# Optimization experiments

Hardware: AMD Instinct MI355X
Metric: run time of the kernel (lower is better)

The kernel has to match this reference:

```python
import math
import jax, jax.numpy as jnp
import numpy as np

NUM_HEADS = 16
QUERY_SIZE = 1024
SEQ = 2048
HEAD = QUERY_SIZE // NUM_HEADS  # qk_size = vo_size = 64


def setup_inputs() -> dict:
    key = jax.random.key(0)
    ks = jax.random.split(key, 8)
    s = 0.02
    query = jax.random.normal(ks[0], (SEQ, QUERY_SIZE), jnp.float32)
    key_ = jax.random.normal(ks[1], (SEQ, QUERY_SIZE), jnp.float32)
    value = jax.random.normal(ks[2], (SEQ, QUERY_SIZE), jnp.float32)
    # causal mask (mask='causal' with state=None -> offset 0)
    mask = jnp.tril(jnp.ones((SEQ, SEQ), dtype=bool))
    Wq = jax.random.normal(ks[3], (QUERY_SIZE, QUERY_SIZE), jnp.float32) * s
    Wk = jax.random.normal(ks[4], (QUERY_SIZE, QUERY_SIZE), jnp.float32) * s
    Wv = jax.random.normal(ks[5], (QUERY_SIZE, QUERY_SIZE), jnp.float32) * s
    Wo = jax.random.normal(ks[6], (QUERY_SIZE, QUERY_SIZE), jnp.float32) * s
    return {"query": query, "key_": key_, "value": value, "mask": mask,
            "Wq": Wq, "Wk": Wk, "Wv": Wv, "Wo": Wo}


def reference(query, key_, value, mask, Wq, Wk, Wv, Wo):
    H, D = NUMS = NUM_HEADS, HEAD
    S = query.shape[0]
    inv_sqrt_d = 1.0 / math.sqrt(D)
    # per-token linear projections, split into heads: [S, H, D]
    q = (query @ Wq.T).reshape(S, H, D)
    k = (key_ @ Wk.T).reshape(S, H, D)
    v = (value @ Wv.T).reshape(S, H, D)
    # NOTE: original divides BOTH q and k by sqrt(d) (effective 1/d scaling)
    q = q * inv_sqrt_d
    k = k * inv_sqrt_d
    # logits per head: [H, S, S]
    logits = jnp.einsum('shd,Shd->hsS', q, k)
    logits = jnp.where(mask[None, :, :], logits, jnp.finfo(logits.dtype).min)
    # per-head GLOBAL max subtraction, softmax in fp32, cast back (faithful)
    m = jnp.max(logits, axis=(1, 2), keepdims=True)
    weights = jax.nn.softmax((logits - m).astype(jnp.float32), axis=-1).astype(query.dtype)
    attn = jnp.einsum('hsS,ShD->shD', weights, v).reshape(S, H * D)
    return attn @ Wo.T
```

## Files before the change

### kernel.cpp

```cpp
#include <hip/hip_runtime.h>
#include <hip/hip_bf16.h>

typedef __bf16 bf16_t;
typedef __bf16 bf16x8 __attribute__((ext_vector_type(8)));
typedef float f32x4 __attribute__((ext_vector_type(4)));

#define MFMA(A, B, C) __builtin_amdgcn_mfma_f32_16x16x32_bf16(A, B, C, 0, 0, 0)

#define GLL16(g, l) __builtin_amdgcn_global_load_lds(                      \
    (const __attribute__((address_space(1))) void*)(g),                    \
    (__attribute__((address_space(3))) void*)(l), 16, 0, 0)

__global__ __launch_bounds__(256) void cvt_all(
    const float* __restrict__ q, const float* __restrict__ k, const float* __restrict__ v,
    const float* __restrict__ wq, const float* __restrict__ wk,
    const float* __restrict__ wv, const float* __restrict__ wo,
    bf16_t* __restrict__ xq, bf16_t* __restrict__ xk, bf16_t* __restrict__ xv,
    bf16_t* __restrict__ ywq, bf16_t* __restrict__ ywk,
    bf16_t* __restrict__ ywv, bf16_t* __restrict__ ywo)
{
  const long gid = (long)blockIdx.x * 256 + threadIdx.x;
  const float* s; bf16_t* d; long off; float sc = 1.0f;
  if (gid < 262144)       { s = q;  d = xq;  off = gid; }
  else if (gid < 524288)  { s = k;  d = xk;  off = gid - 262144; }
  else if (gid < 786432)  { s = v;  d = xv;  off = gid - 524288; }
  else if (gid < 917504)  { s = wq; d = ywq; off = gid - 786432;  sc = 0.125f; }
  else if (gid < 1048576) { s = wk; d = ywk; off = gid - 917504;  sc = 0.125f; }
  else if (gid < 1179648) { s = wv; d = ywv; off = gid - 1048576; }
  else                    { s = wo; d = ywo; off = gid - 1179648; }
  const float* p = s + off * 8;
  float4 a = *(const float4*)p, b = *(const float4*)(p + 4);
  bf16x8 o;
  o[0] = (bf16_t)(a.x * sc); o[1] = (bf16_t)(a.y * sc);
  o[2] = (bf16_t)(a.z * sc); o[3] = (bf16_t)(a.w * sc);
  o[4] = (bf16_t)(b.x * sc); o[5] = (bf16_t)(b.y * sc);
  o[6] = (bf16_t)(b.z * sc); o[7] = (bf16_t)(b.w * sc);
  *(bf16x8*)(d + off * 8) = o;
}

__device__ __forceinline__ void gemm_core(const bf16_t* __restrict__ A,
                                          const bf16_t* __restrict__ W,
                                          int bm, int bn,
                                          bf16_t (&As)[2][128 * 64],
                                          bf16_t (&Bs)[2][64 * 64],
                                          f32x4 (&acc)[4][2])
{
  const int tid = threadIdx.x, lane = tid & 63, wave = tid >> 6;
  const int l15 = lane & 15, l4 = lane >> 4, l7 = l15 & 7;
  const int wm = (wave >> 1) * 64, wn = (wave & 1) * 32;

  auto stage = [&](int buf, int k0) {
#pragma unroll
    for (int i = 0; i < 4; ++i) {
      const int id = i * 256 + tid, row = id >> 3, cph = id & 7;
      GLL16(A + (size_t)(bm + row) * 1024 + k0 + 8 * (cph ^ (row & 7)),
            &As[buf][(i * 256 + wave * 64) * 8]);
    }
#pragma unroll
    for (int i = 0; i < 2; ++i) {
      const int id = i * 256 + tid, row = id >> 3, cph = id & 7;
      GLL16(W + (size_t)(bn + row) * 1024 + k0 + 8 * (cph ^ (row & 7)),
            &Bs[buf][(i * 256 + wave * 64) * 8]);
    }
  };

  stage(0, 0);
#pragma unroll
  for (int s = 0; s < 16; ++s) {
    __syncthreads();
    if (s + 1 < 16) stage((s + 1) & 1, (s + 1) * 64);
    const bf16_t* as = As[s & 1];
    const bf16_t* bs = Bs[s & 1];
#pragma unroll
    for (int ks = 0; ks < 2; ++ks) {
      bf16x8 af[4], bfr[2];
#pragma unroll
      for (int i = 0; i < 4; ++i)
        af[i] = *(const bf16x8*)(&as[(wm + i * 16 + l15) * 64 + 8 * ((ks * 4 + l4) ^ l7)]);
#pragma unroll
      for (int j = 0; j < 2; ++j)
        bfr[j] = *(const bf16x8*)(&bs[(wn + j * 16 + l15) * 64 + 8 * ((ks * 4 + l4) ^ l7)]);
#pragma unroll
      for (int i = 0; i < 4; ++i)
#pragma unroll
        for (int j = 0; j < 2; ++j)
          acc[i][j] = MFMA(af[i], bfr[j], acc[i][j]);
    }
  }
}

__global__ __launch_bounds__(256) void gemm_qkv(
    const bf16_t* __restrict__ xq, const bf16_t* __restrict__ xk, const bf16_t* __restrict__ xv,
    const bf16_t* __restrict__ ywq, const bf16_t* __restrict__ ywk, const bf16_t* __restrict__ ywv,
    bf16_t* __restrict__ qo, bf16_t* __restrict__ ko, bf16_t* __restrict__ vt)
{
  __shared__ __align__(16) bf16_t As[2][128 * 64];
  __shared__ __align__(16) bf16_t Bs[2][64 * 64];
  const int z = blockIdx.z;
  const bf16_t* A = z == 0 ? xq : z == 1 ? xk : xv;
  const bf16_t* W = z == 0 ? ywq : z == 1 ? ywk : ywv;
  const int bm = blockIdx.x * 128, bn = blockIdx.y * 64;
  f32x4 acc[4][2] = {};
  gemm_core(A, W, bm, bn, As, Bs, acc);
  const int tid = threadIdx.x, lane = tid & 63, wave = tid >> 6;
  const int l15 = lane & 15, l4 = lane >> 4;
  const int wm = (wave >> 1) * 64, wn = (wave & 1) * 32;
  if (z < 2) {
    bf16_t* C = z == 0 ? qo : ko;
#pragma unroll
    for (int i = 0; i < 4; ++i)
#pragma unroll
      for (int j = 0; j < 2; ++j)
#pragma unroll
        for (int r = 0; r < 4; ++r)
          C[(size_t)(bm + wm + i * 16 + 4 * l4 + r) * 1024 + bn + wn + j * 16 + l15] =
              (bf16_t)acc[i][j][r];
  } else {
#pragma unroll
    for (int i = 0; i < 4; ++i)
#pragma unroll
      for (int j = 0; j < 2; ++j)
#pragma unroll
        for (int r = 0; r < 4; ++r)
          vt[(size_t)(bn + wn + j * 16 + l15) * 2048 + bm + wm + i * 16 + 4 * l4 + r] =
              (bf16_t)acc[i][j][r];
  }
}

__global__ __launch_bounds__(256) void gemm_out(
    const bf16_t* __restrict__ ctx, const bf16_t* __restrict__ ywo, float* __restrict__ out)
{
  __shared__ __align__(16) bf16_t As[2][128 * 64];
  __shared__ __align__(16) bf16_t Bs[2][64 * 64];
  const int bm = blockIdx.x * 128, bn = blockIdx.y * 64;
  f32x4 acc[4][2] = {};
  gemm_core(ctx, ywo, bm, bn, As, Bs, acc);
  const int tid = threadIdx.x, lane = tid & 63, wave = tid >> 6;
  const int l15 = lane & 15, l4 = lane >> 4;
  const int wm = (wave >> 1) * 64, wn = (wave & 1) * 32;
#pragma unroll
  for (int i = 0; i < 4; ++i)
#pragma unroll
    for (int j = 0; j < 2; ++j)
#pragma unroll
      for (int r = 0; r < 4; ++r)
        out[(size_t)(bm + wm + i * 16 + 4 * l4 + r) * 1024 + bn + wn + j * 16 + l15] =
            acc[i][j][r];
}

__global__ __launch_bounds__(512) void attn512(
    const bf16_t* __restrict__ Qb, const bf16_t* __restrict__ Kb,
    const bf16_t* __restrict__ Vt, bf16_t* __restrict__ Ctx)
{
  __shared__ __align__(16) bf16_t Ks[2][128 * 64];
  __shared__ __align__(16) bf16_t Vs[2][64 * 128];
  __shared__ __align__(16) bf16_t Ps[8][16 * 64];

  const int bid = blockIdx.x;
  const int h = 2 * (bid & 7) + ((bid >> 3) >> 4);
  const int jp = (bid >> 3) & 15;
  const int hoff = h * 64;
  const int tid = threadIdx.x;
  const int lane = tid & 63, wave = tid >> 6;
  const int g = wave & 3, kh = wave >> 2;
  const int l15 = lane & 15, l4 = lane >> 4;
  const int l7 = l15 & 7;

  const int qtA = jp, qtB = 31 - jp;
  const int qbA = qtA * 64, qbB = qtB * 64;
  const int nscA = qtA / 2 + 1, nscB = qtB / 2 + 1;

  const int qrA = qbA + g * 16 + l15, qrB = qbB + g * 16 + l15;
  bf16x8 qA0 = *(const bf16x8*)(Qb + (size_t)qrA * 1024 + hoff + 8 * l4);
  bf16x8 qA1 = *(const bf16x8*)(Qb + (size_t)qrA * 1024 + hoff + 32 + 8 * l4);
  bf16x8 qB0 = *(const bf16x8*)(Qb + (size_t)qrB * 1024 + hoff + 8 * l4);
  bf16x8 qB1 = *(const bf16x8*)(Qb + (size_t)qrB * 1024 + hoff + 32 + 8 * l4);

  f32x4 oA[4] = {}, oB[4] = {};
  float dA[4] = {0.f, 0.f, 0.f, 0.f}, dB[4] = {0.f, 0.f, 0.f, 0.f};

  bf16x8 rk[2], rv[2];
  auto issue = [&](int sc) {
    const int t0 = sc * 128;
#pragma unroll
    for (int i = 0; i < 2; ++i) {
      const int id = tid + 512 * i;
      const int kr = id >> 3, kc = id & 7;
      rk[i] = *(const bf16x8*)(Kb + (size_t)(t0 + kr) * 1024 + hoff + 8 * kc);
      const int vr = id >> 4, vc = id & 15;
      rv[i] = *(const bf16x8*)(Vt + (size_t)(hoff + vr) * 2048 + t0 + 8 * vc);
    }
  };
  auto commit = [&](int buf) {
#pragma unroll
    for (int i = 0; i < 2; ++i) {
      const int id = tid + 512 * i;
      const int kr = id >> 3, kc = id & 7;
      *(bf16x8*)(&Ks[buf][kr * 64 + 8 * (kc ^ (kr & 7))]) = rk[i];
      const int vr = id >> 4, vc = id & 15;
      *(bf16x8*)(&Vs[buf][vr * 128 + 8 * (vc ^ (vr & 7))]) = rv[i];
    }
  };

  auto process = [&](int sc, int cur, int qb, const bf16x8& q0, const bf16x8& q1,
                     f32x4 (&oacc)[4], float (&den)[4]) {
    if (128 * sc + 64 * kh > qb + g * 16 + 15) return;
    const int tb = 128 * sc + 64 * kh;
#pragma unroll
    for (int sub = 0; sub < 4; ++sub) {
      const int krow = 64 * kh + 16 * sub + l15;
      bf16x8 kf0 = *(const bf16x8*)(&Ks[cur][krow * 64 + 8 * (l4 ^ l7)]);
      bf16x8 kf1 = *(const bf16x8*)(&Ks[cur][krow * 64 + 8 * ((4 + l4) ^ l7)]);
      __builtin_amdgcn_s_setprio(1);
      f32x4 sv = {};
      sv = MFMA(q0, kf0, sv);
      sv = MFMA(q1, kf1, sv);
      __builtin_amdgcn_s_setprio(0);
      const int t = tb + 16 * sub + l15;
#pragma unroll
      for (int r = 0; r < 4; ++r) {
        const int qq = qb + g * 16 + 4 * l4 + r;
        const float p = (t <= qq) ? __expf(sv[r]) : 0.0f;
        const bf16_t pb = (bf16_t)p;
        den[r] += (float)pb;
        const int prow = 4 * l4 + r;
        const int pch = 2 * sub + (l15 >> 3);
        Ps[wave][prow * 64 + 8 * (pch ^ (prow & 7)) + l7] = pb;
      }
    }
    asm volatile("s_waitcnt lgkmcnt(0)" ::: "memory");
    __builtin_amdgcn_s_setprio(1);
#pragma unroll
    for (int ks = 0; ks < 2; ++ks) {
      bf16x8 pf = *(const bf16x8*)(&Ps[wave][l15 * 64 + 8 * ((ks * 4 + l4) ^ l7)]);
#pragma unroll
      for (int db = 0; db < 4; ++db) {
        bf16x8 vf = *(const bf16x8*)(&Vs[cur][(db * 16 + l15) * 128 + 64 * kh + 8 * ((ks * 4 + l4) ^ l7)]);
        oacc[db] = MFMA(pf, vf, oacc[db]);
      }
    }
    __builtin_amdgcn_s_setprio(0);
  };

  issue(0);
  commit(0);
  int cur = 0;
  for (int sc = 0; sc < nscB; ++sc) {
    const bool pre = (sc + 1 < nscB);
    __syncthreads();
    if (pre) issue(sc + 1);
    process(sc, cur, qbB, qB0, qB1, oB, dB);
    if (sc < nscA) process(sc, cur, qbA, qA0, qA1, oA, dA);
    if (pre) commit(cur ^ 1);
    cur ^= 1;
  }

  __syncthreads();
#pragma unroll
  for (int r = 0; r < 4; ++r)
#pragma unroll
    for (int m = 1; m < 16; m <<= 1) {
      dA[r] += __shfl_xor(dA[r], m, 64);
      dB[r] += __shfl_xor(dB[r], m, 64);
    }
  float* Os = (float*)(&Ks[0][0]);
  float* Ds = (float*)(&Vs[0][0]);
  if (kh == 1) {
#pragma unroll
    for (int r = 0; r < 4; ++r) {
      const int row = g * 16 + 4 * l4 + r;
#pragma unroll
      for (int db = 0; db < 4; ++db) {
        Os[(0 * 64 + row) * 64 + db * 16 + l15] = oA[db][r];
        Os[(1 * 64 + row) * 64 + db * 16 + l15] = oB[db][r];
      }
      if (l15 == 0) { Ds[0 * 64 + row] = dA[r]; Ds[1 * 64 + row] = dB[r]; }
    }
  }
  __syncthreads();
  if (kh == 0) {
#pragma unroll
    for (int r = 0; r < 4; ++r) {
      const int row = g * 16 + 4 * l4 + r;
      const float iA = 1.0f / (dA[r] + Ds[0 * 64 + row]);
      const float iB = 1.0f / (dB[r] + Ds[1 * 64 + row]);
#pragma unroll
      for (int db = 0; db < 4; ++db) {
        const float vA = oA[db][r] + Os[(0 * 64 + row) * 64 + db * 16 + l15];
        const float vB = oB[db][r] + Os[(1 * 64 + row) * 64 + db * 16 + l15];
        Ctx[(size_t)(qbA + row) * 1024 + hoff + db * 16 + l15] = (bf16_t)(vA * iA);
        Ctx[(size_t)(qbB + row) * 1024 + hoff + db * 16 + l15] = (bf16_t)(vB * iB);
      }
    }
  }
}

extern "C" void kernel_launch(void* const* d_in, const int* in_sizes, int n_in,
                              void* d_out, int out_size, void* d_ws, size_t ws_size,
                              hipStream_t stream)
{
  const float* query = (const float*)d_in[0];
  const float* key_  = (const float*)d_in[1];
  const float* value = (const float*)d_in[2];
  const float* Wq = (const float*)d_in[4];
  const float* Wk = (const float*)d_in[5];
  const float* Wv = (const float*)d_in[6];
  const float* Wo = (const float*)d_in[7];
  float* out = (float*)d_out;

  const size_t SE = (size_t)2048 * 1024, EE = (size_t)1024 * 1024;
  bf16_t* xq  = (bf16_t*)d_ws;
  bf16_t* xk  = xq + SE;
  bf16_t* xv  = xk + SE;
  bf16_t* wq  = xv + SE;
  bf16_t* wk  = wq + EE;
  bf16_t* wv  = wk + EE;
  bf16_t* wo  = wv + EE;
  bf16_t* qo  = wo + EE;
  bf16_t* ko  = qo + SE;
  bf16_t* vt  = ko + SE;
  bf16_t* ctx = vt + SE;

  cvt_all<<<5120, 256, 0, stream>>>(query, key_, value, Wq, Wk, Wv, Wo,
                                    xq, xk, xv, wq, wk, wv, wo);
  gemm_qkv<<<dim3(16, 16, 3), 256, 0, stream>>>(xq, xk, xv, wq, wk, wv, qo, ko, vt);
  attn512<<<256, 512, 0, stream>>>(qo, ko, vt, ctx);
  gemm_out<<<dim3(16, 16), 256, 0, stream>>>(ctx, wo, out);
}
```

Before: 75.64 us.

## Use head-major Q/K/ctx layout and register-streamed attention without shared K/V tiles

Q, K and the attention context are stored head-major ([head][seq][64]) so each head's data is contiguous, and the output GEMM reads ctx in that layout. The attention kernel drops the shared-memory K/V double buffer and barriers. Each wave loads its own 32-key slice of K and V straight into registers, with two register sets alternating to prefetch. The four key-split partial results are combined through shared memory at the end, and the log2(e) factor is folded into Wk so exp2 replaces exp. This removes per-iteration block syncs and LDS staging, at the cost of more registers, uncoalesced per-lane global loads, and a larger final combine.

```diff
diff --git a/kernel.cpp b/kernel.cpp
--- a/kernel.cpp
+++ b/kernel.cpp
@@ -25,7 +25,7 @@
   else if (gid < 524288)  { s = k;  d = xk;  off = gid - 262144; }
   else if (gid < 786432)  { s = v;  d = xv;  off = gid - 524288; }
   else if (gid < 917504)  { s = wq; d = ywq; off = gid - 786432;  sc = 0.125f; }
-  else if (gid < 1048576) { s = wk; d = ywk; off = gid - 917504;  sc = 0.125f; }
+  else if (gid < 1048576) { s = wk; d = ywk; off = gid - 917504;  sc = 0.125f * 1.44269504f; }
   else if (gid < 1179648) { s = wv; d = ywv; off = gid - 1048576; }
   else                    { s = wo; d = ywo; off = gid - 1179648; }
   const float* p = s + off * 8;
@@ -38,6 +38,7 @@
   *(bf16x8*)(d + off * 8) = o;
 }
 
+template<int HM_A>
 __device__ __forceinline__ void gemm_core(const bf16_t* __restrict__ A,
                                           const bf16_t* __restrict__ W,
                                           int bm, int bn,
@@ -53,8 +54,10 @@
 #pragma unroll
     for (int i = 0; i < 4; ++i) {
       const int id = i * 256 + tid, row = id >> 3, cph = id & 7;
-      GLL16(A + (size_t)(bm + row) * 1024 + k0 + 8 * (cph ^ (row & 7)),
-            &As[buf][(i * 256 + wave * 64) * 8]);
+      const size_t asrc = HM_A
+          ? (size_t)(k0 >> 6) * 131072 + (size_t)(bm + row) * 64 + 8 * (cph ^ (row & 7))
+          : (size_t)(bm + row) * 1024 + k0 + 8 * (cph ^ (row & 7));
+      GLL16(A + asrc, &As[buf][(i * 256 + wave * 64) * 8]);
     }
 #pragma unroll
     for (int i = 0; i < 2; ++i) {
@@ -92,7 +95,7 @@
 __global__ __launch_bounds__(256) void gemm_qkv(
     const bf16_t* __restrict__ xq, const bf16_t* __restrict__ xk, const bf16_t* __restrict__ xv,
     const bf16_t* __restrict__ ywq, const bf16_t* __restrict__ ywk, const bf16_t* __restrict__ ywv,
-    bf16_t* __restrict__ qo, bf16_t* __restrict__ ko, bf16_t* __restrict__ vt)
+    bf16_t* __restrict__ qhm, bf16_t* __restrict__ khm, bf16_t* __restrict__ vt)
 {
   __shared__ __align__(16) bf16_t As[2][128 * 64];
   __shared__ __align__(16) bf16_t Bs[2][64 * 64];
@@ -101,19 +104,20 @@
   const bf16_t* W = z == 0 ? ywq : z == 1 ? ywk : ywv;
   const int bm = blockIdx.x * 128, bn = blockIdx.y * 64;
   f32x4 acc[4][2] = {};
-  gemm_core(A, W, bm, bn, As, Bs, acc);
+  gemm_core<0>(A, W, bm, bn, As, Bs, acc);
   const int tid = threadIdx.x, lane = tid & 63, wave = tid >> 6;
   const int l15 = lane & 15, l4 = lane >> 4;
   const int wm = (wave >> 1) * 64, wn = (wave & 1) * 32;
   if (z < 2) {
-    bf16_t* C = z == 0 ? qo : ko;
+    bf16_t* C = z == 0 ? qhm : khm;
+    const size_t hbase = (size_t)(bn >> 6) * 131072;
 #pragma unroll
     for (int i = 0; i < 4; ++i)
 #pragma unroll
       for (int j = 0; j < 2; ++j)
 #pragma unroll
         for (int r = 0; r < 4; ++r)
-          C[(size_t)(bm + wm + i * 16 + 4 * l4 + r) * 1024 + bn + wn + j * 16 + l15] =
+          C[hbase + (size_t)(bm + wm + i * 16 + 4 * l4 + r) * 64 + wn + j * 16 + l15] =
               (bf16_t)acc[i][j][r];
   } else {
 #pragma unroll
@@ -134,7 +138,7 @@
   __shared__ __align__(16) bf16_t Bs[2][64 * 64];
   const int bm = blockIdx.x * 128, bn = blockIdx.y * 64;
   f32x4 acc[4][2] = {};
-  gemm_core(ctx, ywo, bm, bn, As, Bs, acc);
+  gemm_core<1>(ctx, ywo, bm, bn, As, Bs, acc);
   const int tid = threadIdx.x, lane = tid & 63, wave = tid >> 6;
   const int l15 = lane & 15, l4 = lane >> 4;
   const int wm = (wave >> 1) * 64, wn = (wave & 1) * 32;
@@ -148,151 +152,161 @@
             acc[i][j][r];
 }
 
-__global__ __launch_bounds__(512) void attn512(
-    const bf16_t* __restrict__ Qb, const bf16_t* __restrict__ Kb,
-    const bf16_t* __restrict__ Vt, bf16_t* __restrict__ Ctx)
-{
-  __shared__ __align__(16) bf16_t Ks[2][128 * 64];
-  __shared__ __align__(16) bf16_t Vs[2][64 * 128];
-  __shared__ __align__(16) bf16_t Ps[8][16 * 64];
+__global__ __launch_bounds__(512) void attn_nb(
+    const bf16_t* __restrict__ Qh, const bf16_t* __restrict__ Kh,
+    const bf16_t* __restrict__ Vth, bf16_t* __restrict__ Ch)
+{
+  __shared__ __align__(16) bf16_t Ps[8][32 * 40];
+  __shared__ float Ocomb[3][2][32][66];
+  __shared__ float Dcomb[3][2][32];
 
   const int bid = blockIdx.x;
-  const int h = 2 * (bid & 7) + ((bid >> 3) >> 4);
+  const int h = 2 * (bid & 7) + (bid >> 7);
   const int jp = (bid >> 3) & 15;
-  const int hoff = h * 64;
-  const int tid = threadIdx.x;
-  const int lane = tid & 63, wave = tid >> 6;
-  const int g = wave & 3, kh = wave >> 2;
+  const int tid = threadIdx.x, lane = tid & 63, wave = tid >> 6;
+  const int qh = wave & 1, tq = wave >> 1;
   const int l15 = lane & 15, l4 = lane >> 4;
-  const int l7 = l15 & 7;
+
+  const bf16_t* Qb = Qh + (size_t)h * 131072;
+  const bf16_t* Kb = Kh + (size_t)h * 131072;
+  const bf16_t* Vb = Vth + (size_t)h * 131072;
 
   const int qtA = jp, qtB = 31 - jp;
   const int qbA = qtA * 64, qbB = qtB * 64;
-  const int nscA = qtA / 2 + 1, nscB = qtB / 2 + 1;
-
-  const int qrA = qbA + g * 16 + l15, qrB = qbB + g * 16 + l15;
-  bf16x8 qA0 = *(const bf16x8*)(Qb + (size_t)qrA * 1024 + hoff + 8 * l4);
-  bf16x8 qA1 = *(const bf16x8*)(Qb + (size_t)qrA * 1024 + hoff + 32 + 8 * l4);
-  bf16x8 qB0 = *(const bf16x8*)(Qb + (size_t)qrB * 1024 + hoff + 8 * l4);
-  bf16x8 qB1 = *(const bf16x8*)(Qb + (size_t)qrB * 1024 + hoff + 32 + 8 * l4);
-
-  f32x4 oA[4] = {}, oB[4] = {};
-  float dA[4] = {0.f, 0.f, 0.f, 0.f}, dB[4] = {0.f, 0.f, 0.f, 0.f};
-
-  bf16x8 rk[2], rv[2];
-  auto issue = [&](int sc) {
-    const int t0 = sc * 128;
-#pragma unroll
-    for (int i = 0; i < 2; ++i) {
-      const int id = tid + 512 * i;
-      const int kr = id >> 3, kc = id & 7;
-      rk[i] = *(const bf16x8*)(Kb + (size_t)(t0 + kr) * 1024 + hoff + 8 * kc);
-      const int vr = id >> 4, vc = id & 15;
-      rv[i] = *(const bf16x8*)(Vt + (size_t)(hoff + vr) * 2048 + t0 + 8 * vc);
-    }
-  };
-  auto commit = [&](int buf) {
-#pragma unroll
-    for (int i = 0; i < 2; ++i) {
-      const int id = tid + 512 * i;
-      const int kr = id >> 3, kc = id & 7;
-      *(bf16x8*)(&Ks[buf][kr * 64 + 8 * (kc ^ (kr & 7))]) = rk[i];
-      const int vr = id >> 4, vc = id & 15;
-      *(bf16x8*)(&Vs[buf][vr * 128 + 8 * (vc ^ (vr & 7))]) = rv[i];
-    }
-  };
-
-  auto process = [&](int sc, int cur, int qb, const bf16x8& q0, const bf16x8& q1,
-                     f32x4 (&oacc)[4], float (&den)[4]) {
-    if (128 * sc + 64 * kh > qb + g * 16 + 15) return;
-    const int tb = 128 * sc + 64 * kh;
-#pragma unroll
-    for (int sub = 0; sub < 4; ++sub) {
-      const int krow = 64 * kh + 16 * sub + l15;
-      bf16x8 kf0 = *(const bf16x8*)(&Ks[cur][krow * 64 + 8 * (l4 ^ l7)]);
-      bf16x8 kf1 = *(const bf16x8*)(&Ks[cur][krow * 64 + 8 * ((4 + l4) ^ l7)]);
-      __builtin_amdgcn_s_setprio(1);
-      f32x4 sv = {};
-      sv = MFMA(q0, kf0, sv);
-      sv = MFMA(q1, kf1, sv);
-      __builtin_amdgcn_s_setprio(0);
-      const int t = tb + 16 * sub + l15;
-#pragma unroll
-      for (int r = 0; r < 4; ++r) {
-        const int qq = qb + g * 16 + 4 * l4 + r;
-        const float p = (t <= qq) ? __expf(sv[r]) : 0.0f;
-        const bf16_t pb = (bf16_t)p;
-        den[r] += (float)pb;
-        const int prow = 4 * l4 + r;
-        const int pch = 2 * sub + (l15 >> 3);
-        Ps[wave][prow * 64 + 8 * (pch ^ (prow & 7)) + l7] = pb;
+  auto nscw = [&](int qb) {
+    const int lim = qb + 32 * qh + 31 - 32 * tq;
+    return lim < 0 ? 0 : (lim >> 7) + 1;
+  };
+  const int nscAw = nscw(qbA), nscBw = nscw(qbB);
+
+  bf16x8 qA[2][2], qB[2][2];
+#pragma unroll
+  for (int qf = 0; qf < 2; ++qf)
+#pragma unroll
+    for (int kc = 0; kc < 2; ++kc) {
+      qA[qf][kc] = *(const bf16x8*)(Qb + (size_t)(qbA + 32 * qh + 16 * qf + l15) * 64 + kc * 32 + 8 * l4);
+      qB[qf][kc] = *(const bf16x8*)(Qb + (size_t)(qbB + 32 * qh + 16 * qf + l15) * 64 + kc * 32 + 8 * l4);
+    }
+
+  f32x4 oA[2][4] = {}, oB[2][4] = {};
+  float dA[2][4] = {}, dB[2][4] = {};
+
+  struct KVREG { bf16x8 k[2][2]; bf16x8 v[4]; };
+  KVREG kv0, kv1;
+  auto LOADKV = [&](KVREG& kv, int sc) {
+    const int t0w = sc * 128 + tq * 32;
+#pragma unroll
+    for (int tf = 0; tf < 2; ++tf)
+#pragma unroll
+      for (int kc = 0; kc < 2; ++kc)
+        kv.k[tf][kc] = *(const bf16x8*)(Kb + (size_t)(t0w + 16 * tf + l15) * 64 + kc * 32 + 8 * l4);
+#pragma unroll
+    for (int df = 0; df < 4; ++df)
+      kv.v[df] = *(const bf16x8*)(Vb + (size_t)(16 * df + l15) * 2048 + t0w + 8 * l4);
+  };
+
+  bf16_t* Pw = &Ps[wave][0];
+  auto PROC1 = [&](const KVREG& kv, int sc, int qb, const bf16x8 (&qf_)[2][2],
+                   f32x4 (&oacc)[2][4], float (&den)[2][4]) {
+    const int t0w = sc * 128 + tq * 32;
+    f32x4 sv[2][2] = {};
+#pragma unroll
+    for (int qf = 0; qf < 2; ++qf)
+#pragma unroll
+      for (int tf = 0; tf < 2; ++tf) {
+        sv[qf][tf] = MFMA(qf_[qf][0], kv.k[tf][0], sv[qf][tf]);
+        sv[qf][tf] = MFMA(qf_[qf][1], kv.k[tf][1], sv[qf][tf]);
       }
-    }
+#pragma unroll
+    for (int qf = 0; qf < 2; ++qf)
+#pragma unroll
+      for (int tf = 0; tf < 2; ++tf) {
+        const int t = t0w + 16 * tf + l15;
+#pragma unroll
+        for (int r = 0; r < 4; ++r) {
+          const int qq = qb + 32 * qh + 16 * qf + 4 * l4 + r;
+          const float p = (t <= qq) ? __builtin_amdgcn_exp2f(sv[qf][tf][r]) : 0.0f;
+          const bf16_t pb = (bf16_t)p;
+          den[qf][r] += (float)pb;
+          Pw[(16 * qf + 4 * l4 + r) * 40 + 16 * tf + l15] = pb;
+        }
+      }
     asm volatile("s_waitcnt lgkmcnt(0)" ::: "memory");
-    __builtin_amdgcn_s_setprio(1);
-#pragma unroll
-    for (int ks = 0; ks < 2; ++ks) {
-      bf16x8 pf = *(const bf16x8*)(&Ps[wave][l15 * 64 + 8 * ((ks * 4 + l4) ^ l7)]);
-#pragma unroll
-      for (int db = 0; db < 4; ++db) {
-        bf16x8 vf = *(const bf16x8*)(&Vs[cur][(db * 16 + l15) * 128 + 64 * kh + 8 * ((ks * 4 + l4) ^ l7)]);
-        oacc[db] = MFMA(pf, vf, oacc[db]);
+    bf16x8 pa[2];
+#pragma unroll
+    for (int qf = 0; qf < 2; ++qf)
+      pa[qf] = *(const bf16x8*)(&Pw[(16 * qf + l15) * 40 + 8 * l4]);
+#pragma unroll
+    for (int qf = 0; qf < 2; ++qf)
+#pragma unroll
+      for (int df = 0; df < 4; ++df)
+        oacc[qf][df] = MFMA(pa[qf], kv.v[df], oacc[qf][df]);
+  };
+  auto PROC = [&](const KVREG& kv, int sc) {
+    PROC1(kv, sc, qbB, qB, oB, dB);
+    if (sc < nscAw) PROC1(kv, sc, qbA, qA, oA, dA);
+  };
+
+  int sc = 0;
+  LOADKV(kv0, 0);
+  while (sc < nscBw) {
+    if (sc + 1 < nscBw) LOADKV(kv1, sc + 1);
+    PROC(kv0, sc);
+    ++sc;
+    if (sc >= nscBw) break;
+    if (sc + 1 < nscBw) LOADKV(kv0, sc + 1);
+    PROC(kv1, sc);
+    ++sc;
+  }
+
+#pragma unroll
+  for (int qf = 0; qf < 2; ++qf)
+#pragma unroll
+    for (int r = 0; r < 4; ++r)
+#pragma unroll
+      for (int m = 1; m < 16; m <<= 1) {
+        dA[qf][r] += __shfl_xor(dA[qf][r], m, 64);
+        dB[qf][r] += __shfl_xor(dB[qf][r], m, 64);
       }
-    }
-    __builtin_amdgcn_s_setprio(0);
-  };
-
-  issue(0);
-  commit(0);
-  int cur = 0;
-  for (int sc = 0; sc < nscB; ++sc) {
-    const bool pre = (sc + 1 < nscB);
+
+  auto combine = [&](int qb, f32x4 (&oacc)[2][4], float (&den)[2][4]) {
+    if (tq > 0) {
+#pragma unroll
+      for (int qf = 0; qf < 2; ++qf)
+#pragma unroll
+        for (int df = 0; df < 4; ++df)
+#pragma unroll
+          for (int r = 0; r < 4; ++r)
+            Ocomb[tq - 1][qh][16 * qf + 4 * l4 + r][16 * df + l15] = oacc[qf][df][r];
+      if (l15 == 0)
+#pragma unroll
+        for (int qf = 0; qf < 2; ++qf)
+#pragma unroll
+          for (int r = 0; r < 4; ++r)
+            Dcomb[tq - 1][qh][16 * qf + 4 * l4 + r] = den[qf][r];
+    }
     __syncthreads();
-    if (pre) issue(sc + 1);
-    process(sc, cur, qbB, qB0, qB1, oB, dB);
-    if (sc < nscA) process(sc, cur, qbA, qA0, qA1, oA, dA);
-    if (pre) commit(cur ^ 1);
-    cur ^= 1;
-  }
-
-  __syncthreads();
-#pragma unroll
-  for (int r = 0; r < 4; ++r)
-#pragma unroll
-    for (int m = 1; m < 16; m <<= 1) {
-      dA[r] += __shfl_xor(dA[r], m, 64);
-      dB[r] += __shfl_xor(dB[r], m, 64);
-    }
-  float* Os = (float*)(&Ks[0][0]);
-  float* Ds = (float*)(&Vs[0][0]);
-  if (kh == 1) {
-#pragma unroll
-    for (int r = 0; r < 4; ++r) {
-      const int row = g * 16 + 4 * l4 + r;
-#pragma unroll
-      for (int db = 0; db < 4; ++db) {
-        Os[(0 * 64 + row) * 64 + db * 16 + l15] = oA[db][r];
-        Os[(1 * 64 + row) * 64 + db * 16 + l15] = oB[db][r];
-      }
-      if (l15 == 0) { Ds[0 * 64 + row] = dA[r]; Ds[1 * 64 + row] = dB[r]; }
-    }
-  }
-  __syncthreads();
-  if (kh == 0) {
-#pragma unroll
-    for (int r = 0; r < 4; ++r) {
-      const int row = g * 16 + 4 * l4 + r;
-      const float iA = 1.0f / (dA[r] + Ds[0 * 64 + row]);
-      const float iB = 1.0f / (dB[r] + Ds[1 * 64 + row]);
-#pragma unroll
-      for (int db = 0; db < 4; ++db) {
-        const float vA = oA[db][r] + Os[(0 * 64 + row) * 64 + db * 16 + l15];
-        const float vB = oB[db][r] + Os[(1 * 64 + row) * 64 + db * 16 + l15];
-        Ctx[(size_t)(qbA + row) * 1024 + hoff + db * 16 + l15] = (bf16_t)(vA * iA);
-        Ctx[(size_t)(qbB + row) * 1024 + hoff + db * 16 + l15] = (bf16_t)(vB * iB);
-      }
-    }
-  }
+    if (tq == 0) {
+#pragma unroll
+      for (int qf = 0; qf < 2; ++qf)
+#pragma unroll
+        for (int r = 0; r < 4; ++r) {
+          const int row = 16 * qf + 4 * l4 + r;
+          const float dt = den[qf][r] + Dcomb[0][qh][row] + Dcomb[1][qh][row] + Dcomb[2][qh][row];
+          const float inv = 1.0f / dt;
+#pragma unroll
+          for (int df = 0; df < 4; ++df) {
+            const int col = 16 * df + l15;
+            const float s = oacc[qf][df][r] + Ocomb[0][qh][row][col] +
+                            Ocomb[1][qh][row][col] + Ocomb[2][qh][row][col];
+            Ch[(size_t)h * 131072 + (size_t)(qb + 32 * qh + row) * 64 + col] = (bf16_t)(s * inv);
+          }
+        }
+    }
+    __syncthreads();
+  };
+  combine(qbA, oA, dA);
+  combine(qbB, oB, dB);
 }
 
 extern "C" void kernel_launch(void* const* d_in, const int* in_sizes, int n_in,
@@ -316,14 +330,14 @@
   bf16_t* wk  = wq + EE;
   bf16_t* wv  = wk + EE;
   bf16_t* wo  = wv + EE;
-  bf16_t* qo  = wo + EE;
-  bf16_t* ko  = qo + SE;
-  bf16_t* vt  = ko + SE;
+  bf16_t* qhm = wo + EE;
+  bf16_t* khm = qhm + SE;
+  bf16_t* vt  = khm + SE;
   bf16_t* ctx = vt + SE;
 
   cvt_all<<<5120, 256, 0, stream>>>(query, key_, value, Wq, Wk, Wv, Wo,
                                     xq, xk, xv, wq, wk, wv, wo);
-  gemm_qkv<<<dim3(16, 16, 3), 256, 0, stream>>>(xq, xk, xv, wq, wk, wv, qo, ko, vt);
-  attn512<<<256, 512, 0, stream>>>(qo, ko, vt, ctx);
+  gemm_qkv<<<dim3(16, 16, 3), 256, 0, stream>>>(xq, xk, xv, wq, wk, wv, qhm, khm, vt);
+  attn_nb<<<256, 512, 0, stream>>>(qhm, khm, vt, ctx);
   gemm_out<<<dim3(16, 16), 256, 0, stream>>>(ctx, wo, out);
 }
```

Result: slower. 91.06 us (+20.4%).

## Widen attention blocks to 1024 threads with four-way key split per chunk

Applied to the files above, without the earlier changes.

The attention kernel now runs 16 waves per block instead of 8. Each 128-key chunk is split across four key groups of 32 keys rather than two of 64, and the partial outputs and denominators of the four groups are combined through shared memory at the end. The intent is to raise parallelism and latency hiding, since the grid is only 256 blocks. In exchange it adds a heavier final reduction, and per-wave work is smaller, so barrier overhead weighs more. The GEMM core loop also moves its barrier so that staging is issued before the sync, and adds a second barrier after the MFMAs.

```diff
diff --git a/kernel.cpp b/kernel.cpp
--- a/kernel.cpp
+++ b/kernel.cpp
@@ -67,8 +67,8 @@
   stage(0, 0);
 #pragma unroll
   for (int s = 0; s < 16; ++s) {
-    __syncthreads();
     if (s + 1 < 16) stage((s + 1) & 1, (s + 1) * 64);
+    __syncthreads();
     const bf16_t* as = As[s & 1];
     const bf16_t* bs = Bs[s & 1];
 #pragma unroll
@@ -86,6 +86,7 @@
         for (int j = 0; j < 2; ++j)
           acc[i][j] = MFMA(af[i], bfr[j], acc[i][j]);
     }
+    __syncthreads();
   }
 }
 
@@ -148,98 +149,92 @@
             acc[i][j][r];
 }
 
-__global__ __launch_bounds__(512) void attn512(
+__global__ __launch_bounds__(1024) void attn1024(
     const bf16_t* __restrict__ Qb, const bf16_t* __restrict__ Kb,
     const bf16_t* __restrict__ Vt, bf16_t* __restrict__ Ctx)
 {
-  __shared__ __align__(16) bf16_t Ks[2][128 * 64];
-  __shared__ __align__(16) bf16_t Vs[2][64 * 128];
-  __shared__ __align__(16) bf16_t Ps[8][16 * 64];
+  __shared__ __align__(16) char pool[64 * 1024 + 16 * 16 * 40 * 2 + 3 * 64 * 4];
+  bf16_t* KsP = (bf16_t*)pool;
+  bf16_t* VsP = (bf16_t*)(pool + 32 * 1024);
+  bf16_t* PsP = (bf16_t*)(pool + 64 * 1024);
+  float*  Osc = (float*)pool;
+  float*  Dsc = (float*)(pool + 64 * 1024 + 16 * 16 * 40 * 2);
 
   const int bid = blockIdx.x;
-  const int h = 2 * (bid & 7) + ((bid >> 3) >> 4);
+  const int h = 2 * (bid & 7) + (bid >> 7);
   const int jp = (bid >> 3) & 15;
   const int hoff = h * 64;
-  const int tid = threadIdx.x;
-  const int lane = tid & 63, wave = tid >> 6;
-  const int g = wave & 3, kh = wave >> 2;
-  const int l15 = lane & 15, l4 = lane >> 4;
-  const int l7 = l15 & 7;
+  const int tid = threadIdx.x, lane = tid & 63, wave = tid >> 6;
+  const int qg = wave & 3, kh = wave >> 2;
+  const int l15 = lane & 15, l4 = lane >> 4, l7 = l15 & 7;
 
   const int qtA = jp, qtB = 31 - jp;
   const int qbA = qtA * 64, qbB = qtB * 64;
-  const int nscA = qtA / 2 + 1, nscB = qtB / 2 + 1;
-
-  const int qrA = qbA + g * 16 + l15, qrB = qbB + g * 16 + l15;
-  bf16x8 qA0 = *(const bf16x8*)(Qb + (size_t)qrA * 1024 + hoff + 8 * l4);
-  bf16x8 qA1 = *(const bf16x8*)(Qb + (size_t)qrA * 1024 + hoff + 32 + 8 * l4);
-  bf16x8 qB0 = *(const bf16x8*)(Qb + (size_t)qrB * 1024 + hoff + 8 * l4);
-  bf16x8 qB1 = *(const bf16x8*)(Qb + (size_t)qrB * 1024 + hoff + 32 + 8 * l4);
+  const int nscB = qtB / 2 + 1;
+  const int qmaxA = qbA + 16 * qg + 15;
+  const int qmaxB = qbB + 16 * qg + 15;
+
+  bf16x8 qA[2], qB[2];
+#pragma unroll
+  for (int kc = 0; kc < 2; ++kc) {
+    qA[kc] = *(const bf16x8*)(Qb + (size_t)(qbA + 16 * qg + l15) * 1024 + hoff + 32 * kc + 8 * l4);
+    qB[kc] = *(const bf16x8*)(Qb + (size_t)(qbB + 16 * qg + l15) * 1024 + hoff + 32 * kc + 8 * l4);
+  }
 
   f32x4 oA[4] = {}, oB[4] = {};
   float dA[4] = {0.f, 0.f, 0.f, 0.f}, dB[4] = {0.f, 0.f, 0.f, 0.f};
 
-  bf16x8 rk[2], rv[2];
+  bf16x8 rk, rv;
   auto issue = [&](int sc) {
     const int t0 = sc * 128;
-#pragma unroll
-    for (int i = 0; i < 2; ++i) {
-      const int id = tid + 512 * i;
-      const int kr = id >> 3, kc = id & 7;
-      rk[i] = *(const bf16x8*)(Kb + (size_t)(t0 + kr) * 1024 + hoff + 8 * kc);
-      const int vr = id >> 4, vc = id & 15;
-      rv[i] = *(const bf16x8*)(Vt + (size_t)(hoff + vr) * 2048 + t0 + 8 * vc);
-    }
+    const int kr = tid >> 3, kc = tid & 7;
+    rk = *(const bf16x8*)(Kb + (size_t)(t0 + kr) * 1024 + hoff + 8 * kc);
+    const int vr = tid >> 4, vc = tid & 15;
+    rv = *(const bf16x8*)(Vt + (size_t)(hoff + vr) * 2048 + t0 + 8 * vc);
   };
   auto commit = [&](int buf) {
-#pragma unroll
-    for (int i = 0; i < 2; ++i) {
-      const int id = tid + 512 * i;
-      const int kr = id >> 3, kc = id & 7;
-      *(bf16x8*)(&Ks[buf][kr * 64 + 8 * (kc ^ (kr & 7))]) = rk[i];
-      const int vr = id >> 4, vc = id & 15;
-      *(bf16x8*)(&Vs[buf][vr * 128 + 8 * (vc ^ (vr & 7))]) = rv[i];
-    }
-  };
-
-  auto process = [&](int sc, int cur, int qb, const bf16x8& q0, const bf16x8& q1,
-                     f32x4 (&oacc)[4], float (&den)[4]) {
-    if (128 * sc + 64 * kh > qb + g * 16 + 15) return;
-    const int tb = 128 * sc + 64 * kh;
-#pragma unroll
-    for (int sub = 0; sub < 4; ++sub) {
-      const int krow = 64 * kh + 16 * sub + l15;
-      bf16x8 kf0 = *(const bf16x8*)(&Ks[cur][krow * 64 + 8 * (l4 ^ l7)]);
-      bf16x8 kf1 = *(const bf16x8*)(&Ks[cur][krow * 64 + 8 * ((4 + l4) ^ l7)]);
-      __builtin_amdgcn_s_setprio(1);
-      f32x4 sv = {};
-      sv = MFMA(q0, kf0, sv);
-      sv = MFMA(q1, kf1, sv);
-      __builtin_amdgcn_s_setprio(0);
-      const int t = tb + 16 * sub + l15;
+    const int kr = tid >> 3, kc = tid & 7;
+    *(bf16x8*)(&KsP[buf * 8192 + kr * 64 + 8 * (kc ^ (kr & 7))]) = rk;
+    const int vr = tid >> 4, vc = tid & 15;
+    *(bf16x8*)(&VsP[buf * 8192 + vr * 128 + 8 * (vc ^ (vr & 7))]) = rv;
+  };
+
+  bf16_t* Pw = &PsP[wave * 640];
+  auto PROC1 = [&](int cur, int sc, int qb, int qmax, const bf16x8 (&qf)[2],
+                   f32x4 (&oacc)[4], float (&den)[4]) {
+    const int tb = sc * 128 + kh * 32;
+    if (tb > qmax) return;
+    const bf16_t* Ksb = KsP + cur * 8192;
+    const bf16_t* Vsb = VsP + cur * 8192;
+    f32x4 sv[2] = {};
+#pragma unroll
+    for (int tf = 0; tf < 2; ++tf) {
+      const int krow = 32 * kh + 16 * tf + l15;
+      bf16x8 kf0 = *(const bf16x8*)(&Ksb[krow * 64 + 8 * (l4 ^ l7)]);
+      bf16x8 kf1 = *(const bf16x8*)(&Ksb[krow * 64 + 8 * ((4 + l4) ^ l7)]);
+      sv[tf] = MFMA(qf[0], kf0, sv[tf]);
+      sv[tf] = MFMA(qf[1], kf1, sv[tf]);
+    }
+#pragma unroll
+    for (int tf = 0; tf < 2; ++tf) {
+      const int t = tb + 16 * tf + l15;
 #pragma unroll
       for (int r = 0; r < 4; ++r) {
-        const int qq = qb + g * 16 + 4 * l4 + r;
-        const float p = (t <= qq) ? __expf(sv[r]) : 0.0f;
+        const int qq = qb + 16 * qg + 4 * l4 + r;
+        const float p = (t <= qq) ? __expf(sv[tf][r]) : 0.0f;
         const bf16_t pb = (bf16_t)p;
         den[r] += (float)pb;
-        const int prow = 4 * l4 + r;
-        const int pch = 2 * sub + (l15 >> 3);
-        Ps[wave][prow * 64 + 8 * (pch ^ (prow & 7)) + l7] = pb;
+        Pw[(4 * l4 + r) * 40 + 16 * tf + l15] = pb;
       }
     }
     asm volatile("s_waitcnt lgkmcnt(0)" ::: "memory");
-    __builtin_amdgcn_s_setprio(1);
-#pragma unroll
-    for (int ks = 0; ks < 2; ++ks) {
-      bf16x8 pf = *(const bf16x8*)(&Ps[wave][l15 * 64 + 8 * ((ks * 4 + l4) ^ l7)]);
-#pragma unroll
-      for (int db = 0; db < 4; ++db) {
-        bf16x8 vf = *(const bf16x8*)(&Vs[cur][(db * 16 + l15) * 128 + 64 * kh + 8 * ((ks * 4 + l4) ^ l7)]);
-        oacc[db] = MFMA(pf, vf, oacc[db]);
-      }
-    }
-    __builtin_amdgcn_s_setprio(0);
+    bf16x8 pa = *(const bf16x8*)(&Pw[l15 * 40 + 8 * l4]);
+#pragma unroll
+    for (int df = 0; df < 4; ++df) {
+      const int vrow = 16 * df + l15;
+      bf16x8 vf = *(const bf16x8*)(&Vsb[vrow * 128 + 8 * ((4 * kh + l4) ^ l7)]);
+      oacc[df] = MFMA(pa, vf, oacc[df]);
+    }
   };
 
   issue(0);
@@ -247,15 +242,14 @@
   int cur = 0;
   for (int sc = 0; sc < nscB; ++sc) {
     const bool pre = (sc + 1 < nscB);
-    __syncthreads();
     if (pre) issue(sc + 1);
-    process(sc, cur, qbB, qB0, qB1, oB, dB);
-    if (sc < nscA) process(sc, cur, qbA, qA0, qA1, oA, dA);
+    __syncthreads();
+    PROC1(cur, sc, qbB, qmaxB, qB, oB, dB);
+    PROC1(cur, sc, qbA, qmaxA, qA, oA, dA);
     if (pre) commit(cur ^ 1);
     cur ^= 1;
   }
 
-  __syncthreads();
 #pragma unroll
   for (int r = 0; r < 4; ++r)
 #pragma unroll
@@ -263,36 +257,38 @@
       dA[r] += __shfl_xor(dA[r], m, 64);
       dB[r] += __shfl_xor(dB[r], m, 64);
     }
-  float* Os = (float*)(&Ks[0][0]);
-  float* Ds = (float*)(&Vs[0][0]);
-  if (kh == 1) {
-#pragma unroll
-    for (int r = 0; r < 4; ++r) {
-      const int row = g * 16 + 4 * l4 + r;
-#pragma unroll
-      for (int db = 0; db < 4; ++db) {
-        Os[(0 * 64 + row) * 64 + db * 16 + l15] = oA[db][r];
-        Os[(1 * 64 + row) * 64 + db * 16 + l15] = oB[db][r];
+
+  auto combine = [&](int qb, f32x4 (&oacc)[4], float (&den)[4]) {
+    __syncthreads();
+    if (kh > 0) {
+      const int rl = qg * 16 + 4 * l4;
+#pragma unroll
+      for (int r = 0; r < 4; ++r) {
+#pragma unroll
+        for (int df = 0; df < 4; ++df)
+          Osc[((kh - 1) * 64 + rl + r) * 66 + 16 * df + l15] = oacc[df][r];
+        if (l15 == 0) Dsc[(kh - 1) * 64 + rl + r] = den[r];
       }
-      if (l15 == 0) { Ds[0 * 64 + row] = dA[r]; Ds[1 * 64 + row] = dB[r]; }
-    }
-  }
-  __syncthreads();
-  if (kh == 0) {
-#pragma unroll
-    for (int r = 0; r < 4; ++r) {
-      const int row = g * 16 + 4 * l4 + r;
-      const float iA = 1.0f / (dA[r] + Ds[0 * 64 + row]);
-      const float iB = 1.0f / (dB[r] + Ds[1 * 64 + row]);
-#pragma unroll
-      for (int db = 0; db < 4; ++db) {
-        const float vA = oA[db][r] + Os[(0 * 64 + row) * 64 + db * 16 + l15];
-        const float vB = oB[db][r] + Os[(1 * 64 + row) * 64 + db * 16 + l15];
-        Ctx[(size_t)(qbA + row) * 1024 + hoff + db * 16 + l15] = (bf16_t)(vA * iA);
-        Ctx[(size_t)(qbB + row) * 1024 + hoff + db * 16 + l15] = (bf16_t)(vB * iB);
+    }
+    __syncthreads();
+    if (kh == 0) {
+#pragma unroll
+      for (int r = 0; r < 4; ++r) {
+        const int row = qg * 16 + 4 * l4 + r;
+        const float dt = den[r] + Dsc[row] + Dsc[64 + row] + Dsc[128 + row];
+        const float inv = 1.0f / dt;
+#pragma unroll
+        for (int df = 0; df < 4; ++df) {
+          const int col = 16 * df + l15;
+          const float s = oacc[df][r] + Osc[row * 66 + col] +
+                          Osc[(64 + row) * 66 + col] + Osc[(128 + row) * 66 + col];
+          Ctx[(size_t)(qb + row) * 1024 + hoff + col] = (bf16_t)(s * inv);
+        }
       }
     }
-  }
+  };
+  combine(qbA, oA, dA);
+  combine(qbB, oB, dB);
 }
 
 extern "C" void kernel_launch(void* const* d_in, const int* in_sizes, int n_in,
@@ -324,6 +320,6 @@
   cvt_all<<<5120, 256, 0, stream>>>(query, key_, value, Wq, Wk, Wv, Wo,
                                     xq, xk, xv, wq, wk, wv, wo);
   gemm_qkv<<<dim3(16, 16, 3), 256, 0, stream>>>(xq, xk, xv, wq, wk, wv, qo, ko, vt);
-  attn512<<<256, 512, 0, stream>>>(qo, ko, vt, ctx);
+  attn1024<<<256, 1024, 0, stream>>>(qo, ko, vt, ctx);
   gemm_out<<<dim3(16, 16), 256, 0, stream>>>(ctx, wo, out);
 }
```

Result: faster. 71.54 us (-5.4%).
